# Optimization experiments

Measured on AMD Instinct MI355X. Metric: run time of the kernel, lower is better.

## Reference

```python
import jax, jax.numpy as jnp
import numpy as np

D_LOB = 128
D_HAWKES = 32
N_HEADS = 4
HEAD_DIM = D_LOB // N_HEADS
LN_EPS = 1e-5


def setup_inputs() -> dict:
    key = jax.random.key(0)
    ks = jax.random.split(key, 10)
    B, T = 8, 2048
    s = lambda fan_in: 1.0 / np.sqrt(fan_in)
    return {
        "lob": jax.random.normal(ks[0], (B, T, D_LOB), dtype=jnp.float32),
        "hawkes": jax.random.normal(ks[1], (B, T, D_HAWKES), dtype=jnp.float32),
        # hawkes_proj: Linear(d_hawkes, d_lob)
        "Wp": jax.random.uniform(ks[2], (D_LOB, D_HAWKES), jnp.float32, -s(D_HAWKES), s(D_HAWKES)),
        "bp": jnp.zeros((D_LOB,), jnp.float32),
        # MultiheadAttention packed in-projection (3*d_lob, d_lob) and out-projection
        "Win": jax.random.uniform(ks[3], (3 * D_LOB, D_LOB), jnp.float32, -s(D_LOB), s(D_LOB)),
        "bin_": jnp.zeros((3 * D_LOB,), jnp.float32),
        "Wo": jax.random.uniform(ks[4], (D_LOB, D_LOB), jnp.float32, -s(D_LOB), s(D_LOB)),
        "bo": jnp.zeros((D_LOB,), jnp.float32),
        # LayerNorm affine params
        "gamma": jnp.ones((D_LOB,), jnp.float32),
        "beta": jnp.zeros((D_LOB,), jnp.float32),
    }


def reference(lob, hawkes, Wp, bp, Win, bin_, Wo, bo, gamma, beta):
    B, T, _ = lob.shape
    # hawkes_proj
    h = hawkes @ Wp.T + bp  # (B, T, d_lob)
    # packed QKV projection (query=lob, key=value=h)
    q = lob @ Win[:D_LOB].T + bin_[:D_LOB]
    k = h @ Win[D_LOB:2 * D_LOB].T + bin_[D_LOB:2 * D_LOB]
    v = h @ Win[2 * D_LOB:].T + bin_[2 * D_LOB:]
    # split heads -> (B, H, T, hd)
    split = lambda x: x.reshape(B, T, N_HEADS, HEAD_DIM).transpose(0, 2, 1, 3)
    q, k, v = split(q), split(k), split(v)
    scale = 1.0 / np.sqrt(HEAD_DIM).astype(np.float32)
    scores = jnp.einsum("bhqd,bhkd->bhqk", q * scale, k)  # (B, H, T, T)
    attn = jax.nn.softmax(scores, axis=-1)
    # dropout(p=0.1) omitted: reference is eval/inference mode
    ctx = jnp.einsum("bhqk,bhkd->bhqd", attn, v)  # (B, H, T, hd)
    ctx = ctx.transpose(0, 2, 1, 3).reshape(B, T, D_LOB)
    fused = ctx @ Wo.T + bo
    # residual + LayerNorm
    x = lob + fused
    mu = jnp.mean(x, axis=-1, keepdims=True)
    var = jnp.mean(jnp.square(x - mu), axis=-1, keepdims=True)
    out = (x - mu) * jax.lax.rsqrt(var + LN_EPS) * gamma + beta
    attn_w = jnp.mean(attn, axis=1)  # average over heads (B, T, T)
    return out, attn_w
```

## Files before the change

### kernel.cpp

```cpp
#include <hip/hip_runtime.h>
#include <hip/hip_bf16.h>
#include <math.h>

#define TT 2048
#define BB 8
#define DD 128
#define HH 4
#define BT (BB*TT)
#define BH (BB*HH)
#define SCALE 0.1767766952966369f
#define S2LOG (SCALE * 1.4426950408889634f)

typedef __attribute__((ext_vector_type(8))) short short8;
typedef __attribute__((ext_vector_type(4))) short short4v;
typedef __attribute__((ext_vector_type(4))) float f32x4;
typedef __attribute__((ext_vector_type(4))) unsigned u32x4;
typedef __hip_bfloat16 bf16;

#define MFMA16(a,b,c) __builtin_amdgcn_mfma_f32_16x16x32_bf16(a,b,c,0,0,0)

static __device__ inline short8 ldg8(const bf16* p) {
  return *reinterpret_cast<const short8*>(p);
}
static __device__ inline short4v ldg4(const bf16* p) {
  return *reinterpret_cast<const short4v*>(p);
}
static __device__ inline short f2bs(float x) {
  bf16 h = __float2bfloat16(x);
  return *reinterpret_cast<short*>(&h);
}
static __device__ inline unsigned cvtpk(float lo, float hi) {
  unsigned r;
  asm("v_cvt_pk_bf16_f32 %0, %1, %2" : "=v"(r) : "v"(lo), "v"(hi));
  return r;
}
static __device__ inline short8 ldcvt8(const float* p) {
  f32x4 f0 = *reinterpret_cast<const f32x4*>(p);
  f32x4 f1 = *reinterpret_cast<const f32x4*>(p + 4);
  short8 r;
  #pragma unroll
  for (int i = 0; i < 4; ++i) { r[i] = f2bs(f0[i]); r[4+i] = f2bs(f1[i]); }
  return r;
}

__global__ __launch_bounds__(256) void proj_kernel(
    const float* __restrict__ lob, const float* __restrict__ hawkes,
    const float* __restrict__ Wp, const float* __restrict__ bp,
    const float* __restrict__ Win, const float* __restrict__ binp,
    bf16* __restrict__ qg, bf16* __restrict__ kg, bf16* __restrict__ vtg) {
  __shared__ bf16 hT[32*136];
  __shared__ bf16 sK[32*136];
  __shared__ bf16 vT[128*40];
  int tid = threadIdx.x;
  int wave = tid >> 6, lane = tid & 63;
  int lr = lane & 15, lq = lane >> 4;
  int r0 = blockIdx.x * 32;
  int b  = r0 >> 11, t0 = r0 & 2047;
  f32x4 z = {0.f,0.f,0.f,0.f};

  short8 alob[2][4], ahk[2];
  #pragma unroll
  for (int mt = 0; mt < 2; ++mt) {
    const float* lp = lob + (size_t)(r0 + mt*16 + lr)*128;
    #pragma unroll
    for (int kt = 0; kt < 4; ++kt) alob[mt][kt] = ldcvt8(lp + kt*32 + lq*8);
    ahk[mt] = ldcvt8(hawkes + (size_t)(r0 + mt*16 + lr)*32 + lq*8);
  }

  for (int nt = wave; nt < 8; nt += 4) {
    int cn = nt*16;
    short8 bfrag = ldcvt8(Wp + (size_t)(cn + lr)*32 + lq*8);
    float bias = bp[cn + lr];
    #pragma unroll
    for (int mt = 0; mt < 2; ++mt) {
      f32x4 c = MFMA16(ahk[mt], bfrag, z);
      #pragma unroll
      for (int r = 0; r < 4; ++r)
        hT[(mt*16 + lq*4 + r)*136 + cn + lr] = __float2bfloat16(c[r] + bias);
    }
  }
  __syncthreads();

  short8 ah[2][4];
  #pragma unroll
  for (int mt = 0; mt < 2; ++mt)
    #pragma unroll
    for (int kt = 0; kt < 4; ++kt)
      ah[mt][kt] = *reinterpret_cast<const short8*>(&hT[(mt*16 + lr)*136 + kt*32 + lq*8]);
  __syncthreads();

  for (int nt = wave; nt < 24; nt += 4) {
    int which = nt >> 3;
    int c = (nt & 7)*16 + lr;
    const float* wrow = Win + (size_t)(which*128 + c)*128;
    float bias = binp[which*128 + c];
    f32x4 acc0 = z, acc1 = z;
    #pragma unroll
    for (int kt = 0; kt < 4; ++kt) {
      short8 bfrag = ldcvt8(wrow + kt*32 + lq*8);
      if (which == 0) {
        acc0 = MFMA16(alob[0][kt], bfrag, acc0);
        acc1 = MFMA16(alob[1][kt], bfrag, acc1);
      } else {
        acc0 = MFMA16(ah[0][kt], bfrag, acc0);
        acc1 = MFMA16(ah[1][kt], bfrag, acc1);
      }
    }
    #pragma unroll
    for (int mt = 0; mt < 2; ++mt) {
      f32x4 acc = mt ? acc1 : acc0;
      #pragma unroll
      for (int r = 0; r < 4; ++r) {
        int row = mt*16 + lq*4 + r;
        float val = acc[r] + bias;
        if (which == 0)      hT[row*136 + c] = __float2bfloat16(val);
        else if (which == 1) sK[row*136 + c] = __float2bfloat16(val);
        else                 vT[c*40 + row]  = __float2bfloat16(val);
      }
    }
  }
  __syncthreads();

  {
    int head = tid >> 6, tt = (tid >> 1) & 31, half = tid & 1;
    const bf16* sq = &hT[tt*136 + head*32 + half*16];
    const bf16* sk = &sK[tt*136 + head*32 + half*16];
    bf16* qdst = qg + ((size_t)(b*HH + head)*TT + t0 + tt)*32 + half*16;
    bf16* kdst = kg + ((size_t)(b*HH + head)*TT + t0 + tt)*32 + half*16;
    *reinterpret_cast<short8*>(qdst)     = *reinterpret_cast<const short8*>(sq);
    *reinterpret_cast<short8*>(qdst + 8) = *reinterpret_cast<const short8*>(sq + 8);
    *reinterpret_cast<short8*>(kdst)     = *reinterpret_cast<const short8*>(sk);
    *reinterpret_cast<short8*>(kdst + 8) = *reinterpret_cast<const short8*>(sk + 8);
  }
  {
    int dd = tid >> 1, half = tid & 1;
    int bh = b*HH + (dd >> 5);
    short8 s0 = *reinterpret_cast<const short8*>(&vT[dd*40 + half*16]);
    short8 s1 = *reinterpret_cast<const short8*>(&vT[dd*40 + half*16 + 8]);
    bf16* dst = vtg + ((size_t)bh*32 + (dd & 31))*TT + t0 + half*16;
    *reinterpret_cast<short8*>(dst) = s0;
    *reinterpret_cast<short8*>(dst + 8) = s1;
  }
}

__global__ __launch_bounds__(256) void attn_kernel(const bf16* __restrict__ qg,
    const bf16* __restrict__ kg, const bf16* __restrict__ vtg,
    float* __restrict__ attn_out, const float* __restrict__ lobf,
    const float* __restrict__ Wo, const float* __restrict__ bo,
    const float* __restrict__ gamma, const float* __restrict__ beta,
    float* __restrict__ outg) {
  int wgid = (blockIdx.x & 7)*64 + (blockIdx.x >> 3);
  int b = wgid >> 6, qt = wgid & 63;
  int tid = threadIdx.x;
  int head = tid >> 6, lane = tid & 63;
  int lr = lane & 15, lq = lane >> 4;
  int bh = b*HH + head;
  __shared__ float plds[2][4][32*36];
  const bf16* qp = qg + ((size_t)bh*TT + (size_t)qt*32)*32;
  const bf16* kb = kg + (size_t)bh*TT*32;
  const bf16* vb = vtg + (size_t)bh*32*TT;
  f32x4 z = {0.f,0.f,0.f,0.f};

  short8 aq0 = ldg8(qp + lr*32 + lq*8);
  short8 aq1 = ldg8(qp + (16+lr)*32 + lq*8);

  float rs0 = 0.f, rs1 = 0.f;
  {
    short8 kA0 = ldg8(kb + (size_t)lr*32 + lq*8);
    short8 kA1 = ldg8(kb + (size_t)(16+lr)*32 + lq*8);
    short8 kB0, kB1;
#define P1STEP(KC0, KC1, KN0, KN1, NCC) { \
    int nc_ = (NCC); \
    KN0 = ldg8(kb + (size_t)(nc_*32 + lr)*32 + lq*8); \
    KN1 = ldg8(kb + (size_t)(nc_*32 + 16 + lr)*32 + lq*8); \
    f32x4 sa0 = MFMA16(KC0, aq0, z), sb0 = MFMA16(KC1, aq0, z); \
    f32x4 sa1 = MFMA16(KC0, aq1, z), sb1 = MFMA16(KC1, aq1, z); \
    _Pragma("unroll") for (int r = 0; r < 4; ++r) { \
      rs0 += exp2f(sa0[r]*S2LOG) + exp2f(sb0[r]*S2LOG); \
      rs1 += exp2f(sa1[r]*S2LOG) + exp2f(sb1[r]*S2LOG); } }
    #pragma unroll 1
    for (int c = 0; c < 64; c += 2) {
      P1STEP(kA0, kA1, kB0, kB1, c+1);
      P1STEP(kB0, kB1, kA0, kA1, (c+2 < 64) ? c+2 : 0);
    }
#undef P1STEP
  }
  rs0 += __shfl_xor(rs0, 16, 64); rs0 += __shfl_xor(rs0, 32, 64);
  rs1 += __shfl_xor(rs1, 16, 64); rs1 += __shfl_xor(rs1, 32, 64);
  float lb0 = -log2f(rs0);
  float lb1 = -log2f(rs1);

  f32x4 acc00 = z, acc01 = z, acc10 = z, acc11 = z;
  float* awr = attn_out + (size_t)(b*TT + qt*32)*TT;
  int mq = tid >> 3, mk = (tid & 7)*4;

  short8 kA0 = ldg8(kb + (size_t)lr*32 + lq*8);
  short8 kA1 = ldg8(kb + (size_t)(16+lr)*32 + lq*8);
  short4v vA00 = ldg4(vb + (size_t)lr*TT + lq*4);
  short4v vA01 = ldg4(vb + (size_t)lr*TT + 16 + lq*4);
  short4v vA10 = ldg4(vb + (size_t)(16+lr)*TT + lq*4);
  short4v vA11 = ldg4(vb + (size_t)(16+lr)*TT + 16 + lq*4);
  short8 kB0, kB1; short4v vB00, vB01, vB10, vB11;

#define P2STEP(KC, KC0, KC1, VC00, VC01, VC10, VC11, KN0, KN1, VN00, VN01, VN10, VN11, NCC) { \
    int kc_ = (KC); int nc_ = (NCC); int pb_ = kc_ & 1; \
    KN0 = ldg8(kb + (size_t)(nc_*32 + lr)*32 + lq*8); \
    KN1 = ldg8(kb + (size_t)(nc_*32 + 16 + lr)*32 + lq*8); \
    VN00 = ldg4(vb + (size_t)lr*TT + nc_*32 + lq*4); \
    VN01 = ldg4(vb + (size_t)lr*TT + nc_*32 + 16 + lq*4); \
    VN10 = ldg4(vb + (size_t)(16+lr)*TT + nc_*32 + lq*4); \
    VN11 = ldg4(vb + (size_t)(16+lr)*TT + nc_*32 + 16 + lq*4); \
    f32x4 s00 = MFMA16(KC0, aq0, z), s10 = MFMA16(KC1, aq0, z); \
    f32x4 s01 = MFMA16(KC0, aq1, z), s11 = MFMA16(KC1, aq1, z); \
    f32x4 p00, p10, p01, p11; \
    _Pragma("unroll") for (int r = 0; r < 4; ++r) { \
      p00[r] = exp2f(fmaf(s00[r], S2LOG, lb0)); \
      p10[r] = exp2f(fmaf(s10[r], S2LOG, lb0)); \
      p01[r] = exp2f(fmaf(s01[r], S2LOG, lb1)); \
      p11[r] = exp2f(fmaf(s11[r], S2LOG, lb1)); } \
    { float* pw = &plds[pb_][head][0]; \
      *reinterpret_cast<f32x4*>(pw + lr*36 + lq*4)           = p00; \
      *reinterpret_cast<f32x4*>(pw + lr*36 + 16 + lq*4)      = p10; \
      *reinterpret_cast<f32x4*>(pw + (16+lr)*36 + lq*4)      = p01; \
      *reinterpret_cast<f32x4*>(pw + (16+lr)*36 + 16 + lq*4) = p11; } \
    u32x4 ua_, ub_; \
    ua_[0] = cvtpk(p00[0], p00[1]); ua_[1] = cvtpk(p00[2], p00[3]); \
    ua_[2] = cvtpk(p10[0], p10[1]); ua_[3] = cvtpk(p10[2], p10[3]); \
    ub_[0] = cvtpk(p01[0], p01[1]); ub_[1] = cvtpk(p01[2], p01[3]); \
    ub_[2] = cvtpk(p11[0], p11[1]); ub_[3] = cvtpk(p11[2], p11[3]); \
    short8 ap0 = *reinterpret_cast<short8*>(&ua_); \
    short8 ap1 = *reinterpret_cast<short8*>(&ub_); \
    __syncthreads(); \
    { const float* pr = &plds[pb_][0][0]; \
      f32x4 mv = *reinterpret_cast<const f32x4*>(pr + mq*36 + mk); \
      mv = mv + *reinterpret_cast<const f32x4*>(pr + 1152 + mq*36 + mk); \
      mv = mv + *reinterpret_cast<const f32x4*>(pr + 2304 + mq*36 + mk); \
      mv = mv + *reinterpret_cast<const f32x4*>(pr + 3456 + mq*36 + mk); \
      *reinterpret_cast<f32x4*>(awr + (size_t)mq*TT + kc_*32 + mk) = mv * 0.25f; } \
    short8 vf0, vf1; \
    _Pragma("unroll") for (int j = 0; j < 4; ++j) { \
      vf0[j] = VC00[j]; vf0[4+j] = VC01[j]; \
      vf1[j] = VC10[j]; vf1[4+j] = VC11[j]; } \
    acc00 = MFMA16(ap0, vf0, acc00); acc01 = MFMA16(ap0, vf1, acc01); \
    acc10 = MFMA16(ap1, vf0, acc10); acc11 = MFMA16(ap1, vf1, acc11); }

  #pragma unroll 1
  for (int c = 0; c < 64; c += 2) {
    P2STEP(c,   kA0, kA1, vA00, vA01, vA10, vA11,
                kB0, kB1, vB00, vB01, vB10, vB11, c+1);
    P2STEP(c+1, kB0, kB1, vB00, vB01, vB10, vB11,
                kA0, kA1, vA00, vA01, vA10, vA11, (c+2 < 64) ? c+2 : 0);
  }
#undef P2STEP

  __syncthreads();
  size_t rowbase = (size_t)(b*TT) + (size_t)qt*32;
  float* sX  = &plds[0][0][0];
  float* sX2 = &plds[1][0][0];
  #pragma unroll
  for (int m = 0; m < 2; ++m) {
    f32x4 a0 = m ? acc10 : acc00;
    f32x4 a1 = m ? acc11 : acc01;
    #pragma unroll
    for (int r = 0; r < 4; ++r) {
      int row = m*16 + lq*4 + r;
      sX[row*132 + head*32 + lr]      = a0[r];
      sX[row*132 + head*32 + 16 + lr] = a1[r];
    }
  }
  __syncthreads();
  short8 actx[2][4];
  #pragma unroll
  for (int mt = 0; mt < 2; ++mt)
    #pragma unroll
    for (int kt = 0; kt < 4; ++kt) {
      const float* cp = &sX[(mt*16 + lr)*132 + kt*32 + lq*8];
      f32x4 c0 = *reinterpret_cast<const f32x4*>(cp);
      f32x4 c1 = *reinterpret_cast<const f32x4*>(cp + 4);
      u32x4 u;
      u[0] = cvtpk(c0[0], c0[1]); u[1] = cvtpk(c0[2], c0[3]);
      u[2] = cvtpk(c1[0], c1[1]); u[3] = cvtpk(c1[2], c1[3]);
      actx[mt][kt] = *reinterpret_cast<short8*>(&u);
    }
  for (int nt = head; nt < 8; nt += 4) {
    f32x4 acc0 = z, acc1 = z;
    #pragma unroll
    for (int kt = 0; kt < 4; ++kt) {
      short8 bfrag = ldcvt8(Wo + (size_t)(nt*16 + lr)*128 + kt*32 + lq*8);
      acc0 = MFMA16(actx[0][kt], bfrag, acc0);
      acc1 = MFMA16(actx[1][kt], bfrag, acc1);
    }
    int d = nt*16 + lr;
    float bias = bo[d];
    #pragma unroll
    for (int mt = 0; mt < 2; ++mt) {
      f32x4 acc = mt ? acc1 : acc0;
      #pragma unroll
      for (int r = 0; r < 4; ++r) {
        int row = mt*16 + lq*4 + r;
        sX2[row*132 + d] = acc[r] + bias + lobf[(rowbase + row)*128 + d];
      }
    }
  }
  __syncthreads();
  {
    int row = tid >> 3, j = tid & 7;
    const float* xp = &sX2[row*132 + j*16];
    f32x4 x[4];
    #pragma unroll
    for (int v = 0; v < 4; ++v) x[v] = *reinterpret_cast<const f32x4*>(xp + v*4);
    float sum = 0.f, sq = 0.f;
    #pragma unroll
    for (int v = 0; v < 4; ++v)
      #pragma unroll
      for (int e = 0; e < 4; ++e) { sum += x[v][e]; sq += x[v][e]*x[v][e]; }
    #pragma unroll
    for (int mdx = 1; mdx < 8; mdx <<= 1) {
      sum += __shfl_xor(sum, mdx, 64);
      sq  += __shfl_xor(sq,  mdx, 64);
    }
    float mu = sum * (1.0f/128.0f);
    float rstd = rsqrtf(sq*(1.0f/128.0f) - mu*mu + 1e-5f);
    float* op = outg + (rowbase + row)*128 + j*16;
    #pragma unroll
    for (int v = 0; v < 4; ++v) {
      f32x4 o;
      #pragma unroll
      for (int e = 0; e < 4; ++e) {
        int d = j*16 + v*4 + e;
        o[e] = (x[v][e] - mu)*rstd*gamma[d] + beta[d];
      }
      *reinterpret_cast<f32x4*>(op + v*4) = o;
    }
  }
}

extern "C" void kernel_launch(void* const* d_in, const int* in_sizes, int n_in,
                              void* d_out, int out_size, void* d_ws, size_t ws_size,
                              hipStream_t stream) {
  const float* lob    = (const float*)d_in[0];
  const float* hawkes = (const float*)d_in[1];
  const float* Wp     = (const float*)d_in[2];
  const float* bp     = (const float*)d_in[3];
  const float* Win    = (const float*)d_in[4];
  const float* binp   = (const float*)d_in[5];
  const float* Wo     = (const float*)d_in[6];
  const float* bo     = (const float*)d_in[7];
  const float* gamma  = (const float*)d_in[8];
  const float* beta   = (const float*)d_in[9];
  float* outg = (float*)d_out;
  float* attn_out = outg + (size_t)BT*128;

  char* ws = (char*)d_ws;
  bf16*  qg   = (bf16*)(ws);
  bf16*  kg   = (bf16*)(ws + (size_t)4*1024*1024);
  bf16*  vtg  = (bf16*)(ws + (size_t)8*1024*1024);

  proj_kernel<<<BT/32, 256, 0, stream>>>(lob, hawkes, Wp, bp, Win, binp, qg, kg, vtg);
  attn_kernel<<<BB*(TT/32), 256, 0, stream>>>(qg, kg, vtg, attn_out,
                                              lob, Wo, bo, gamma, beta, outg);
}
```

Measured before the change: 278.4 us.

## Split attention key range across two wave groups per block

```diff
diff --git a/kernel.cpp b/kernel.cpp
--- a/kernel.cpp
+++ b/kernel.cpp
@@ -143,7 +143,7 @@
   }
 }
 
-__global__ __launch_bounds__(256) void attn_kernel(const bf16* __restrict__ qg,
+__global__ __launch_bounds__(512) void attn_kernel(const bf16* __restrict__ qg,
     const bf16* __restrict__ kg, const bf16* __restrict__ vtg,
     float* __restrict__ attn_out, const float* __restrict__ lobf,
     const float* __restrict__ Wo, const float* __restrict__ bo,
@@ -152,7 +152,8 @@
   int wgid = (blockIdx.x & 7)*64 + (blockIdx.x >> 3);
   int b = wgid >> 6, qt = wgid & 63;
   int tid = threadIdx.x;
-  int head = tid >> 6, lane = tid & 63;
+  int wave = tid >> 6, lane = tid & 63;
+  int head = wave & 3, half = wave >> 2;
   int lr = lane & 15, lq = lane >> 4;
   int bh = b*HH + head;
   __shared__ float plds[2][4][32*36];
@@ -166,8 +167,8 @@
 
   float rs0 = 0.f, rs1 = 0.f;
   {
-    short8 kA0 = ldg8(kb + (size_t)lr*32 + lq*8);
-    short8 kA1 = ldg8(kb + (size_t)(16+lr)*32 + lq*8);
+    short8 kA0 = ldg8(kb + (size_t)(half*32 + lr)*32 + lq*8);
+    short8 kA1 = ldg8(kb + (size_t)(half*32 + 16 + lr)*32 + lq*8);
     short8 kB0, kB1;
 #define P1STEP(KC0, KC1, KN0, KN1, NCC) { \
     int nc_ = (NCC); \
@@ -179,31 +180,36 @@
       rs0 += exp2f(sa0[r]*S2LOG) + exp2f(sb0[r]*S2LOG); \
       rs1 += exp2f(sa1[r]*S2LOG) + exp2f(sb1[r]*S2LOG); } }
     #pragma unroll 1
-    for (int c = 0; c < 64; c += 2) {
-      P1STEP(kA0, kA1, kB0, kB1, c+1);
-      P1STEP(kB0, kB1, kA0, kA1, (c+2 < 64) ? c+2 : 0);
+    for (int i = 0; i < 32; i += 2) {
+      P1STEP(kA0, kA1, kB0, kB1, 2*(i+1) + half);
+      P1STEP(kB0, kB1, kA0, kA1, (i+2 < 32) ? 2*(i+2) + half : half);
     }
 #undef P1STEP
   }
   rs0 += __shfl_xor(rs0, 16, 64); rs0 += __shfl_xor(rs0, 32, 64);
   rs1 += __shfl_xor(rs1, 16, 64); rs1 += __shfl_xor(rs1, 32, 64);
-  float lb0 = -log2f(rs0);
-  float lb1 = -log2f(rs1);
+  float* sdl = &plds[0][0][0];
+  if (lq == 0) { sdl[wave*32 + lr] = rs0; sdl[wave*32 + 16 + lr] = rs1; }
+  __syncthreads();
+  float lb0 = -log2f(sdl[head*32 + lr]      + sdl[(4+head)*32 + lr]);
+  float lb1 = -log2f(sdl[head*32 + 16 + lr] + sdl[(4+head)*32 + 16 + lr]);
+  __syncthreads();
 
   f32x4 acc00 = z, acc01 = z, acc10 = z, acc11 = z;
   float* awr = attn_out + (size_t)(b*TT + qt*32)*TT;
-  int mq = tid >> 3, mk = (tid & 7)*4;
-
-  short8 kA0 = ldg8(kb + (size_t)lr*32 + lq*8);
-  short8 kA1 = ldg8(kb + (size_t)(16+lr)*32 + lq*8);
-  short4v vA00 = ldg4(vb + (size_t)lr*TT + lq*4);
-  short4v vA01 = ldg4(vb + (size_t)lr*TT + 16 + lq*4);
-  short4v vA10 = ldg4(vb + (size_t)(16+lr)*TT + lq*4);
-  short4v vA11 = ldg4(vb + (size_t)(16+lr)*TT + 16 + lq*4);
+  int mloc = tid & 255;
+  int mq = mloc >> 3, mk = (mloc & 7)*4;
+
+  short8 kA0 = ldg8(kb + (size_t)(half*32 + lr)*32 + lq*8);
+  short8 kA1 = ldg8(kb + (size_t)(half*32 + 16 + lr)*32 + lq*8);
+  short4v vA00 = ldg4(vb + (size_t)lr*TT + half*32 + lq*4);
+  short4v vA01 = ldg4(vb + (size_t)lr*TT + half*32 + 16 + lq*4);
+  short4v vA10 = ldg4(vb + (size_t)(16+lr)*TT + half*32 + lq*4);
+  short4v vA11 = ldg4(vb + (size_t)(16+lr)*TT + half*32 + 16 + lq*4);
   short8 kB0, kB1; short4v vB00, vB01, vB10, vB11;
 
 #define P2STEP(KC, KC0, KC1, VC00, VC01, VC10, VC11, KN0, KN1, VN00, VN01, VN10, VN11, NCC) { \
-    int kc_ = (KC); int nc_ = (NCC); int pb_ = kc_ & 1; \
+    int kc_ = (KC); int nc_ = (NCC); \
     KN0 = ldg8(kb + (size_t)(nc_*32 + lr)*32 + lq*8); \
     KN1 = ldg8(kb + (size_t)(nc_*32 + 16 + lr)*32 + lq*8); \
     VN00 = ldg4(vb + (size_t)lr*TT + nc_*32 + lq*4); \
@@ -218,7 +224,7 @@
       p10[r] = exp2f(fmaf(s10[r], S2LOG, lb0)); \
       p01[r] = exp2f(fmaf(s01[r], S2LOG, lb1)); \
       p11[r] = exp2f(fmaf(s11[r], S2LOG, lb1)); } \
-    { float* pw = &plds[pb_][head][0]; \
+    { float* pw = &plds[half][head][0]; \
       *reinterpret_cast<f32x4*>(pw + lr*36 + lq*4)           = p00; \
       *reinterpret_cast<f32x4*>(pw + lr*36 + 16 + lq*4)      = p10; \
       *reinterpret_cast<f32x4*>(pw + (16+lr)*36 + lq*4)      = p01; \
@@ -231,7 +237,7 @@
     short8 ap0 = *reinterpret_cast<short8*>(&ua_); \
     short8 ap1 = *reinterpret_cast<short8*>(&ub_); \
     __syncthreads(); \
-    { const float* pr = &plds[pb_][0][0]; \
+    { const float* pr = &plds[half][0][0]; \
       f32x4 mv = *reinterpret_cast<const f32x4*>(pr + mq*36 + mk); \
       mv = mv + *reinterpret_cast<const f32x4*>(pr + 1152 + mq*36 + mk); \
       mv = mv + *reinterpret_cast<const f32x4*>(pr + 2304 + mq*36 + mk); \
@@ -242,33 +248,42 @@
       vf0[j] = VC00[j]; vf0[4+j] = VC01[j]; \
       vf1[j] = VC10[j]; vf1[4+j] = VC11[j]; } \
     acc00 = MFMA16(ap0, vf0, acc00); acc01 = MFMA16(ap0, vf1, acc01); \
-    acc10 = MFMA16(ap1, vf0, acc10); acc11 = MFMA16(ap1, vf1, acc11); }
+    acc10 = MFMA16(ap1, vf0, acc10); acc11 = MFMA16(ap1, vf1, acc11); \
+    __syncthreads(); }
 
   #pragma unroll 1
-  for (int c = 0; c < 64; c += 2) {
-    P2STEP(c,   kA0, kA1, vA00, vA01, vA10, vA11,
-                kB0, kB1, vB00, vB01, vB10, vB11, c+1);
-    P2STEP(c+1, kB0, kB1, vB00, vB01, vB10, vB11,
-                kA0, kA1, vA00, vA01, vA10, vA11, (c+2 < 64) ? c+2 : 0);
+  for (int i = 0; i < 32; i += 2) {
+    P2STEP(2*i + half, kA0, kA1, vA00, vA01, vA10, vA11,
+           kB0, kB1, vB00, vB01, vB10, vB11, 2*(i+1) + half);
+    P2STEP(2*(i+1) + half, kB0, kB1, vB00, vB01, vB10, vB11,
+           kA0, kA1, vA00, vA01, vA10, vA11, (i+2 < 32) ? 2*(i+2) + half : half);
   }
 #undef P2STEP
 
-  __syncthreads();
   size_t rowbase = (size_t)(b*TT) + (size_t)qt*32;
-  float* sX  = &plds[0][0][0];
-  float* sX2 = &plds[1][0][0];
-  #pragma unroll
-  for (int m = 0; m < 2; ++m) {
-    f32x4 a0 = m ? acc10 : acc00;
-    f32x4 a1 = m ? acc11 : acc01;
-    #pragma unroll
-    for (int r = 0; r < 4; ++r) {
-      int row = m*16 + lq*4 + r;
-      sX[row*132 + head*32 + lr]      = a0[r];
-      sX[row*132 + head*32 + 16 + lr] = a1[r];
-    }
-  }
-  __syncthreads();
+  float* sRed = &plds[0][0][0];
+  {
+    float* myR = sRed + half*4224;
+    #pragma unroll
+    for (int m = 0; m < 2; ++m) {
+      f32x4 a0 = m ? acc10 : acc00;
+      f32x4 a1 = m ? acc11 : acc01;
+      #pragma unroll
+      for (int r = 0; r < 4; ++r) {
+        int row = m*16 + lq*4 + r;
+        myR[row*132 + head*32 + lr]      = a0[r];
+        myR[row*132 + head*32 + 16 + lr] = a1[r];
+      }
+    }
+  }
+  __syncthreads();
+  for (int idx = tid; idx < 4096; idx += 512) {
+    int row = idx >> 7, d = idx & 127;
+    sRed[row*132 + d] += sRed[4224 + row*132 + d];
+  }
+  __syncthreads();
+  float* sX  = sRed;
+  float* sX2 = sRed + 4224;
   short8 actx[2][4];
   #pragma unroll
   for (int mt = 0; mt < 2; ++mt)
@@ -282,7 +297,8 @@
       u[2] = cvtpk(c1[0], c1[1]); u[3] = cvtpk(c1[2], c1[3]);
       actx[mt][kt] = *reinterpret_cast<short8*>(&u);
     }
-  for (int nt = head; nt < 8; nt += 4) {
+  {
+    int nt = wave;
     f32x4 acc0 = z, acc1 = z;
     #pragma unroll
     for (int kt = 0; kt < 4; ++kt) {
@@ -304,34 +320,33 @@
   }
   __syncthreads();
   {
-    int row = tid >> 3, j = tid & 7;
-    const float* xp = &sX2[row*132 + j*16];
-    f32x4 x[4];
-    #pragma unroll
-    for (int v = 0; v < 4; ++v) x[v] = *reinterpret_cast<const f32x4*>(xp + v*4);
+    int row = tid >> 4, j = tid & 15;
+    const float* xp = &sX2[row*132 + j*8];
+    f32x4 x0 = *reinterpret_cast<const f32x4*>(xp);
+    f32x4 x1 = *reinterpret_cast<const f32x4*>(xp + 4);
     float sum = 0.f, sq = 0.f;
     #pragma unroll
-    for (int v = 0; v < 4; ++v)
-      #pragma unroll
-      for (int e = 0; e < 4; ++e) { sum += x[v][e]; sq += x[v][e]*x[v][e]; }
-    #pragma unroll
-    for (int mdx = 1; mdx < 8; mdx <<= 1) {
+    for (int e = 0; e < 4; ++e) {
+      sum += x0[e] + x1[e];
+      sq  += x0[e]*x0[e] + x1[e]*x1[e];
+    }
+    #pragma unroll
+    for (int mdx = 1; mdx < 16; mdx <<= 1) {
       sum += __shfl_xor(sum, mdx, 64);
       sq  += __shfl_xor(sq,  mdx, 64);
     }
     float mu = sum * (1.0f/128.0f);
     float rstd = rsqrtf(sq*(1.0f/128.0f) - mu*mu + 1e-5f);
-    float* op = outg + (rowbase + row)*128 + j*16;
-    #pragma unroll
-    for (int v = 0; v < 4; ++v) {
-      f32x4 o;
-      #pragma unroll
-      for (int e = 0; e < 4; ++e) {
-        int d = j*16 + v*4 + e;
-        o[e] = (x[v][e] - mu)*rstd*gamma[d] + beta[d];
-      }
-      *reinterpret_cast<f32x4*>(op + v*4) = o;
-    }
+    float* op = outg + (rowbase + row)*128 + j*8;
+    f32x4 o0, o1;
+    #pragma unroll
+    for (int e = 0; e < 4; ++e) {
+      int d = j*8 + e;
+      o0[e] = (x0[e] - mu)*rstd*gamma[d]   + beta[d];
+      o1[e] = (x1[e] - mu)*rstd*gamma[d+4] + beta[d+4];
+    }
+    *reinterpret_cast<f32x4*>(op)     = o0;
+    *reinterpret_cast<f32x4*>(op + 4) = o1;
   }
 }
 
@@ -357,6 +372,6 @@
   bf16*  vtg  = (bf16*)(ws + (size_t)8*1024*1024);
 
   proj_kernel<<<BT/32, 256, 0, stream>>>(lob, hawkes, Wp, bp, Win, binp, qg, kg, vtg);
-  attn_kernel<<<BB*(TT/32), 256, 0, stream>>>(qg, kg, vtg, attn_out,
+  attn_kernel<<<BB*(TT/32), 512, 0, stream>>>(qg, kg, vtg, attn_out,
                                               lob, Wo, bo, gamma, beta, outg);
 }
```

New measurement: 275.6 us. Within noise of the previous version (-1.0%).

## Split attention key chunks across waves instead of heads to drop per-chunk barriers

Applied to the files above, without the earlier changes.

```diff
diff --git a/kernel.cpp b/kernel.cpp
--- a/kernel.cpp
+++ b/kernel.cpp
@@ -143,6 +143,9 @@
   }
 }
 
+#define KOFF(KC,H) ((size_t)(H)*TT*32 + (size_t)(KC)*1024)
+#define VOFF(KC,H) ((size_t)(H)*32*TT + (size_t)(KC)*32)
+
 __global__ __launch_bounds__(256) void attn_kernel(const bf16* __restrict__ qg,
     const bf16* __restrict__ kg, const bf16* __restrict__ vtg,
     float* __restrict__ attn_out, const float* __restrict__ lobf,
@@ -152,77 +155,105 @@
   int wgid = (blockIdx.x & 7)*64 + (blockIdx.x >> 3);
   int b = wgid >> 6, qt = wgid & 63;
   int tid = threadIdx.x;
-  int head = tid >> 6, lane = tid & 63;
+  int wave = tid >> 6, lane = tid & 63;
   int lr = lane & 15, lq = lane >> 4;
-  int bh = b*HH + head;
-  __shared__ float plds[2][4][32*36];
-  const bf16* qp = qg + ((size_t)bh*TT + (size_t)qt*32)*32;
-  const bf16* kb = kg + (size_t)bh*TT*32;
-  const bf16* vb = vtg + (size_t)bh*32*TT;
+  __shared__ float smem[8448];
+  const bf16* kb0 = kg + (size_t)(b*HH)*TT*32;
+  const bf16* vb0 = vtg + (size_t)(b*HH)*32*TT;
   f32x4 z = {0.f,0.f,0.f,0.f};
 
-  short8 aq0 = ldg8(qp + lr*32 + lq*8);
-  short8 aq1 = ldg8(qp + (16+lr)*32 + lq*8);
-
-  float rs0 = 0.f, rs1 = 0.f;
-  {
-    short8 kA0 = ldg8(kb + (size_t)lr*32 + lq*8);
-    short8 kA1 = ldg8(kb + (size_t)(16+lr)*32 + lq*8);
-    short8 kB0, kB1;
-#define P1STEP(KC0, KC1, KN0, KN1, NCC) { \
-    int nc_ = (NCC); \
-    KN0 = ldg8(kb + (size_t)(nc_*32 + lr)*32 + lq*8); \
-    KN1 = ldg8(kb + (size_t)(nc_*32 + 16 + lr)*32 + lq*8); \
-    f32x4 sa0 = MFMA16(KC0, aq0, z), sb0 = MFMA16(KC1, aq0, z); \
-    f32x4 sa1 = MFMA16(KC0, aq1, z), sb1 = MFMA16(KC1, aq1, z); \
+  short8 aq[4][2];
+  #pragma unroll
+  for (int h = 0; h < 4; ++h)
+    #pragma unroll
+    for (int m = 0; m < 2; ++m)
+      aq[h][m] = ldg8(qg + ((size_t)(b*HH + h)*TT + qt*32 + m*16 + lr)*32 + lq*8);
+
+  float rs[4][2] = {{0.f,0.f},{0.f,0.f},{0.f,0.f},{0.f,0.f}};
+  short8 kA0, kA1, kB0, kB1;
+  kA0 = ldg8(kb0 + KOFF(wave,0) + lr*32 + lq*8);
+  kA1 = ldg8(kb0 + KOFF(wave,0) + (16+lr)*32 + lq*8);
+
+#define H1BODY(RS0, RS1, AQ0, AQ1, KC0, KC1, KN0, KN1, NKOFF) { \
+    KN0 = ldg8(kb0 + (NKOFF) + lr*32 + lq*8); \
+    KN1 = ldg8(kb0 + (NKOFF) + (16+lr)*32 + lq*8); \
+    f32x4 s00 = MFMA16(KC0, AQ0, z), s10 = MFMA16(KC1, AQ0, z); \
+    f32x4 s01 = MFMA16(KC0, AQ1, z), s11 = MFMA16(KC1, AQ1, z); \
     _Pragma("unroll") for (int r = 0; r < 4; ++r) { \
-      rs0 += exp2f(sa0[r]*S2LOG) + exp2f(sb0[r]*S2LOG); \
-      rs1 += exp2f(sa1[r]*S2LOG) + exp2f(sb1[r]*S2LOG); } }
-    #pragma unroll 1
-    for (int c = 0; c < 64; c += 2) {
-      P1STEP(kA0, kA1, kB0, kB1, c+1);
-      P1STEP(kB0, kB1, kA0, kA1, (c+2 < 64) ? c+2 : 0);
-    }
-#undef P1STEP
-  }
-  rs0 += __shfl_xor(rs0, 16, 64); rs0 += __shfl_xor(rs0, 32, 64);
-  rs1 += __shfl_xor(rs1, 16, 64); rs1 += __shfl_xor(rs1, 32, 64);
-  float lb0 = -log2f(rs0);
-  float lb1 = -log2f(rs1);
-
-  f32x4 acc00 = z, acc01 = z, acc10 = z, acc11 = z;
+      RS0 += exp2f(s00[r]*S2LOG) + exp2f(s10[r]*S2LOG); \
+      RS1 += exp2f(s01[r]*S2LOG) + exp2f(s11[r]*S2LOG); } }
+
+  #pragma unroll 1
+  for (int i = 0; i < 16; ++i) {
+    int kc = wave + i*4;
+    int kn = (i < 15) ? kc + 4 : wave;
+    H1BODY(rs[0][0], rs[0][1], aq[0][0], aq[0][1], kA0, kA1, kB0, kB1, KOFF(kc,1));
+    H1BODY(rs[1][0], rs[1][1], aq[1][0], aq[1][1], kB0, kB1, kA0, kA1, KOFF(kc,2));
+    H1BODY(rs[2][0], rs[2][1], aq[2][0], aq[2][1], kA0, kA1, kB0, kB1, KOFF(kc,3));
+    H1BODY(rs[3][0], rs[3][1], aq[3][0], aq[3][1], kB0, kB1, kA0, kA1, KOFF(kn,0));
+  }
+#undef H1BODY
+
+  #pragma unroll
+  for (int h = 0; h < 4; ++h)
+    #pragma unroll
+    for (int m = 0; m < 2; ++m) {
+      rs[h][m] += __shfl_xor(rs[h][m], 16, 64);
+      rs[h][m] += __shfl_xor(rs[h][m], 32, 64);
+    }
+  if (lq == 0) {
+    #pragma unroll
+    for (int h = 0; h < 4; ++h)
+      #pragma unroll
+      for (int m = 0; m < 2; ++m)
+        smem[wave*128 + h*32 + m*16 + lr] = rs[h][m];
+  }
+  __syncthreads();
+  float lb[4][2];
+  #pragma unroll
+  for (int h = 0; h < 4; ++h)
+    #pragma unroll
+    for (int m = 0; m < 2; ++m)
+      lb[h][m] = -log2f(smem[0*128 + h*32 + m*16 + lr] + smem[1*128 + h*32 + m*16 + lr]
+                      + smem[2*128 + h*32 + m*16 + lr] + smem[3*128 + h*32 + m*16 + lr]);
+  __syncthreads();
+
+  f32x4 acc[4][2][2];
+  #pragma unroll
+  for (int h = 0; h < 4; ++h)
+    #pragma unroll
+    for (int m = 0; m < 2; ++m)
+      #pragma unroll
+      for (int dt = 0; dt < 2; ++dt) acc[h][m][dt] = z;
+  f32x4 aw00 = z, aw01 = z, aw10 = z, aw11 = z;
+  float* Sw = smem + wave*1152;
   float* awr = attn_out + (size_t)(b*TT + qt*32)*TT;
-  int mq = tid >> 3, mk = (tid & 7)*4;
-
-  short8 kA0 = ldg8(kb + (size_t)lr*32 + lq*8);
-  short8 kA1 = ldg8(kb + (size_t)(16+lr)*32 + lq*8);
-  short4v vA00 = ldg4(vb + (size_t)lr*TT + lq*4);
-  short4v vA01 = ldg4(vb + (size_t)lr*TT + 16 + lq*4);
-  short4v vA10 = ldg4(vb + (size_t)(16+lr)*TT + lq*4);
-  short4v vA11 = ldg4(vb + (size_t)(16+lr)*TT + 16 + lq*4);
-  short8 kB0, kB1; short4v vB00, vB01, vB10, vB11;
-
-#define P2STEP(KC, KC0, KC1, VC00, VC01, VC10, VC11, KN0, KN1, VN00, VN01, VN10, VN11, NCC) { \
-    int kc_ = (KC); int nc_ = (NCC); int pb_ = kc_ & 1; \
-    KN0 = ldg8(kb + (size_t)(nc_*32 + lr)*32 + lq*8); \
-    KN1 = ldg8(kb + (size_t)(nc_*32 + 16 + lr)*32 + lq*8); \
-    VN00 = ldg4(vb + (size_t)lr*TT + nc_*32 + lq*4); \
-    VN01 = ldg4(vb + (size_t)lr*TT + nc_*32 + 16 + lq*4); \
-    VN10 = ldg4(vb + (size_t)(16+lr)*TT + nc_*32 + lq*4); \
-    VN11 = ldg4(vb + (size_t)(16+lr)*TT + nc_*32 + 16 + lq*4); \
-    f32x4 s00 = MFMA16(KC0, aq0, z), s10 = MFMA16(KC1, aq0, z); \
-    f32x4 s01 = MFMA16(KC0, aq1, z), s11 = MFMA16(KC1, aq1, z); \
+
+  short4v vA00, vA01, vA10, vA11, vB00, vB01, vB10, vB11;
+  kA0 = ldg8(kb0 + KOFF(wave,0) + lr*32 + lq*8);
+  kA1 = ldg8(kb0 + KOFF(wave,0) + (16+lr)*32 + lq*8);
+  vA00 = ldg4(vb0 + VOFF(wave,0) + (size_t)lr*TT + lq*4);
+  vA01 = ldg4(vb0 + VOFF(wave,0) + (size_t)lr*TT + 16 + lq*4);
+  vA10 = ldg4(vb0 + VOFF(wave,0) + (size_t)(16+lr)*TT + lq*4);
+  vA11 = ldg4(vb0 + VOFF(wave,0) + (size_t)(16+lr)*TT + 16 + lq*4);
+
+#define HBODY(ACCH, LB0, LB1, AQ0, AQ1, KC0, KC1, VC00, VC01, VC10, VC11, \
+              KN0, KN1, VN00, VN01, VN10, VN11, NKOFF, NVOFF) { \
+    KN0 = ldg8(kb0 + (NKOFF) + lr*32 + lq*8); \
+    KN1 = ldg8(kb0 + (NKOFF) + (16+lr)*32 + lq*8); \
+    VN00 = ldg4(vb0 + (NVOFF) + (size_t)lr*TT + lq*4); \
+    VN01 = ldg4(vb0 + (NVOFF) + (size_t)lr*TT + 16 + lq*4); \
+    VN10 = ldg4(vb0 + (NVOFF) + (size_t)(16+lr)*TT + lq*4); \
+    VN11 = ldg4(vb0 + (NVOFF) + (size_t)(16+lr)*TT + 16 + lq*4); \
+    f32x4 s00 = MFMA16(KC0, AQ0, z), s10 = MFMA16(KC1, AQ0, z); \
+    f32x4 s01 = MFMA16(KC0, AQ1, z), s11 = MFMA16(KC1, AQ1, z); \
     f32x4 p00, p10, p01, p11; \
     _Pragma("unroll") for (int r = 0; r < 4; ++r) { \
-      p00[r] = exp2f(fmaf(s00[r], S2LOG, lb0)); \
-      p10[r] = exp2f(fmaf(s10[r], S2LOG, lb0)); \
-      p01[r] = exp2f(fmaf(s01[r], S2LOG, lb1)); \
-      p11[r] = exp2f(fmaf(s11[r], S2LOG, lb1)); } \
-    { float* pw = &plds[pb_][head][0]; \
-      *reinterpret_cast<f32x4*>(pw + lr*36 + lq*4)           = p00; \
-      *reinterpret_cast<f32x4*>(pw + lr*36 + 16 + lq*4)      = p10; \
-      *reinterpret_cast<f32x4*>(pw + (16+lr)*36 + lq*4)      = p01; \
-      *reinterpret_cast<f32x4*>(pw + (16+lr)*36 + 16 + lq*4) = p11; } \
+      p00[r] = exp2f(fmaf(s00[r], S2LOG, LB0)); \
+      p10[r] = exp2f(fmaf(s10[r], S2LOG, LB0)); \
+      p01[r] = exp2f(fmaf(s01[r], S2LOG, LB1)); \
+      p11[r] = exp2f(fmaf(s11[r], S2LOG, LB1)); } \
+    aw00 += p00; aw01 += p10; aw10 += p01; aw11 += p11; \
     u32x4 ua_, ub_; \
     ua_[0] = cvtpk(p00[0], p00[1]); ua_[1] = cvtpk(p00[2], p00[3]); \
     ua_[2] = cvtpk(p10[0], p10[1]); ua_[3] = cvtpk(p10[2], p10[3]); \
@@ -230,43 +261,73 @@
     ub_[2] = cvtpk(p11[0], p11[1]); ub_[3] = cvtpk(p11[2], p11[3]); \
     short8 ap0 = *reinterpret_cast<short8*>(&ua_); \
     short8 ap1 = *reinterpret_cast<short8*>(&ub_); \
-    __syncthreads(); \
-    { const float* pr = &plds[pb_][0][0]; \
-      f32x4 mv = *reinterpret_cast<const f32x4*>(pr + mq*36 + mk); \
-      mv = mv + *reinterpret_cast<const f32x4*>(pr + 1152 + mq*36 + mk); \
-      mv = mv + *reinterpret_cast<const f32x4*>(pr + 2304 + mq*36 + mk); \
-      mv = mv + *reinterpret_cast<const f32x4*>(pr + 3456 + mq*36 + mk); \
-      *reinterpret_cast<f32x4*>(awr + (size_t)mq*TT + kc_*32 + mk) = mv * 0.25f; } \
     short8 vf0, vf1; \
     _Pragma("unroll") for (int j = 0; j < 4; ++j) { \
       vf0[j] = VC00[j]; vf0[4+j] = VC01[j]; \
       vf1[j] = VC10[j]; vf1[4+j] = VC11[j]; } \
-    acc00 = MFMA16(ap0, vf0, acc00); acc01 = MFMA16(ap0, vf1, acc01); \
-    acc10 = MFMA16(ap1, vf0, acc10); acc11 = MFMA16(ap1, vf1, acc11); }
+    ACCH[0][0] = MFMA16(ap0, vf0, ACCH[0][0]); \
+    ACCH[0][1] = MFMA16(ap0, vf1, ACCH[0][1]); \
+    ACCH[1][0] = MFMA16(ap1, vf0, ACCH[1][0]); \
+    ACCH[1][1] = MFMA16(ap1, vf1, ACCH[1][1]); }
 
   #pragma unroll 1
-  for (int c = 0; c < 64; c += 2) {
-    P2STEP(c,   kA0, kA1, vA00, vA01, vA10, vA11,
-                kB0, kB1, vB00, vB01, vB10, vB11, c+1);
-    P2STEP(c+1, kB0, kB1, vB00, vB01, vB10, vB11,
-                kA0, kA1, vA00, vA01, vA10, vA11, (c+2 < 64) ? c+2 : 0);
-  }
-#undef P2STEP
+  for (int i = 0; i < 16; ++i) {
+    int kc = wave + i*4;
+    int kn = (i < 15) ? kc + 4 : wave;
+    HBODY(acc[0], lb[0][0], lb[0][1], aq[0][0], aq[0][1],
+          kA0, kA1, vA00, vA01, vA10, vA11,
+          kB0, kB1, vB00, vB01, vB10, vB11, KOFF(kc,1), VOFF(kc,1));
+    HBODY(acc[1], lb[1][0], lb[1][1], aq[1][0], aq[1][1],
+          kB0, kB1, vB00, vB01, vB10, vB11,
+          kA0, kA1, vA00, vA01, vA10, vA11, KOFF(kc,2), VOFF(kc,2));
+    HBODY(acc[2], lb[2][0], lb[2][1], aq[2][0], aq[2][1],
+          kA0, kA1, vA00, vA01, vA10, vA11,
+          kB0, kB1, vB00, vB01, vB10, vB11, KOFF(kc,3), VOFF(kc,3));
+    HBODY(acc[3], lb[3][0], lb[3][1], aq[3][0], aq[3][1],
+          kB0, kB1, vB00, vB01, vB10, vB11,
+          kA0, kA1, vA00, vA01, vA10, vA11, KOFF(kn,0), VOFF(kn,0));
+    *reinterpret_cast<f32x4*>(&Sw[lr*36 + lq*4])           = aw00 * 0.25f;
+    *reinterpret_cast<f32x4*>(&Sw[lr*36 + 16 + lq*4])      = aw01 * 0.25f;
+    *reinterpret_cast<f32x4*>(&Sw[(16+lr)*36 + lq*4])      = aw10 * 0.25f;
+    *reinterpret_cast<f32x4*>(&Sw[(16+lr)*36 + 16 + lq*4]) = aw11 * 0.25f;
+    #pragma unroll
+    for (int g = 0; g < 4; ++g) {
+      int row = g*8 + (lane >> 3), col = (lane & 7)*4;
+      *reinterpret_cast<f32x4*>(awr + (size_t)row*TT + kc*32 + col) =
+          *reinterpret_cast<const f32x4*>(&Sw[row*36 + col]);
+    }
+    aw00 = z; aw01 = z; aw10 = z; aw11 = z;
+  }
+#undef HBODY
 
   __syncthreads();
   size_t rowbase = (size_t)(b*TT) + (size_t)qt*32;
-  float* sX  = &plds[0][0][0];
-  float* sX2 = &plds[1][0][0];
-  #pragma unroll
-  for (int m = 0; m < 2; ++m) {
-    f32x4 a0 = m ? acc10 : acc00;
-    f32x4 a1 = m ? acc11 : acc01;
-    #pragma unroll
-    for (int r = 0; r < 4; ++r) {
-      int row = m*16 + lq*4 + r;
-      sX[row*132 + head*32 + lr]      = a0[r];
-      sX[row*132 + head*32 + 16 + lr] = a1[r];
-    }
+  float* sRed0 = smem;
+  float* sRed1 = smem + 4224;
+  if (wave < 2) {
+    float* myR = (wave == 0) ? sRed0 : sRed1;
+    #pragma unroll
+    for (int h = 0; h < 4; ++h)
+      #pragma unroll
+      for (int m = 0; m < 2; ++m)
+        #pragma unroll
+        for (int dt = 0; dt < 2; ++dt)
+          #pragma unroll
+          for (int r = 0; r < 4; ++r)
+            myR[(m*16 + lq*4 + r)*132 + h*32 + dt*16 + lr] = acc[h][m][dt][r];
+  }
+  __syncthreads();
+  if (wave >= 2) {
+    float* myR = (wave == 2) ? sRed0 : sRed1;
+    #pragma unroll
+    for (int h = 0; h < 4; ++h)
+      #pragma unroll
+      for (int m = 0; m < 2; ++m)
+        #pragma unroll
+        for (int dt = 0; dt < 2; ++dt)
+          #pragma unroll
+          for (int r = 0; r < 4; ++r)
+            myR[(m*16 + lq*4 + r)*132 + h*32 + dt*16 + lr] += acc[h][m][dt][r];
   }
   __syncthreads();
   short8 actx[2][4];
@@ -274,31 +335,37 @@
   for (int mt = 0; mt < 2; ++mt)
     #pragma unroll
     for (int kt = 0; kt < 4; ++kt) {
-      const float* cp = &sX[(mt*16 + lr)*132 + kt*32 + lq*8];
-      f32x4 c0 = *reinterpret_cast<const f32x4*>(cp);
-      f32x4 c1 = *reinterpret_cast<const f32x4*>(cp + 4);
+      int off = (mt*16 + lr)*132 + kt*32 + lq*8;
+      f32x4 c0 = *reinterpret_cast<const f32x4*>(&sRed0[off])
+               + *reinterpret_cast<const f32x4*>(&sRed1[off]);
+      f32x4 c1 = *reinterpret_cast<const f32x4*>(&sRed0[off + 4])
+               + *reinterpret_cast<const f32x4*>(&sRed1[off + 4]);
       u32x4 u;
       u[0] = cvtpk(c0[0], c0[1]); u[1] = cvtpk(c0[2], c0[3]);
       u[2] = cvtpk(c1[0], c1[1]); u[3] = cvtpk(c1[2], c1[3]);
       actx[mt][kt] = *reinterpret_cast<short8*>(&u);
     }
-  for (int nt = head; nt < 8; nt += 4) {
-    f32x4 acc0 = z, acc1 = z;
+  __syncthreads();
+  float* sX2 = smem;
+  #pragma unroll
+  for (int t = 0; t < 2; ++t) {
+    int nt = wave + t*4;
+    f32x4 a0 = z, a1 = z;
     #pragma unroll
     for (int kt = 0; kt < 4; ++kt) {
       short8 bfrag = ldcvt8(Wo + (size_t)(nt*16 + lr)*128 + kt*32 + lq*8);
-      acc0 = MFMA16(actx[0][kt], bfrag, acc0);
-      acc1 = MFMA16(actx[1][kt], bfrag, acc1);
+      a0 = MFMA16(actx[0][kt], bfrag, a0);
+      a1 = MFMA16(actx[1][kt], bfrag, a1);
     }
     int d = nt*16 + lr;
     float bias = bo[d];
     #pragma unroll
-    for (int mt = 0; mt < 2; ++mt) {
-      f32x4 acc = mt ? acc1 : acc0;
+    for (int m = 0; m < 2; ++m) {
+      f32x4 a = m ? a1 : a0;
       #pragma unroll
       for (int r = 0; r < 4; ++r) {
-        int row = mt*16 + lq*4 + r;
-        sX2[row*132 + d] = acc[r] + bias + lobf[(rowbase + row)*128 + d];
+        int row = m*16 + lq*4 + r;
+        sX2[row*132 + d] = a[r] + bias + lobf[(rowbase + row)*128 + d];
       }
     }
   }
```

Result: slower. 305.7 us (+9.8%).
